# Optimization experiments

Hardware: AMD Instinct MI355X
Metric: run time of the kernel (lower is better)

The kernel has to match this reference:

```python
import jax, jax.numpy as jnp
import numpy as np

B, S, D = 8, 1024, 1024
H = 16
DH = D // H
DFF = 4096
L = 2
EPS = 1e-6


def setup_inputs() -> dict:
    key = jax.random.key(0)
    ks = jax.random.split(key, 12)
    sc = 0.02
    x = jax.random.normal(ks[0], (B, S, D), dtype=jnp.float32)
    # causal mask: 1 where position j > i (masked), broadcast over batch/head
    mask = jnp.triu(jnp.ones((S, S), dtype=jnp.float32), k=1)[None, None]
    Wq = jax.random.normal(ks[1], (L, D, D), dtype=jnp.float32) * sc
    Wk = jax.random.normal(ks[2], (L, D, D), dtype=jnp.float32) * sc
    Wv = jax.random.normal(ks[3], (L, D, D), dtype=jnp.float32) * sc
    Wo = jax.random.normal(ks[4], (L, D, D), dtype=jnp.float32) * sc
    bq = jnp.zeros((L, D), jnp.float32)
    bk = jnp.zeros((L, D), jnp.float32)
    bv = jnp.zeros((L, D), jnp.float32)
    bo = jnp.zeros((L, D), jnp.float32)
    W1 = jax.random.normal(ks[5], (L, D, DFF), dtype=jnp.float32) * sc
    b1 = jnp.zeros((L, DFF), jnp.float32)
    W2 = jax.random.normal(ks[6], (L, DFF, D), dtype=jnp.float32) * sc
    b2 = jnp.zeros((L, D), jnp.float32)
    ln1_g = jnp.ones((L, D), jnp.float32)
    ln1_b = jnp.zeros((L, D), jnp.float32)
    ln2_g = jnp.ones((L, D), jnp.float32)
    ln2_b = jnp.zeros((L, D), jnp.float32)
    return dict(x=x, mask=mask, Wq=Wq, bq=bq, Wk=Wk, bk=bk, Wv=Wv, bv=bv,
                Wo=Wo, bo=bo, W1=W1, b1=b1, W2=W2, b2=b2,
                ln1_g=ln1_g, ln1_b=ln1_b, ln2_g=ln2_g, ln2_b=ln2_b)


def layer_norm(x, g, b):
    mu = jnp.mean(x, axis=-1, keepdims=True)
    var = jnp.mean(jnp.square(x - mu), axis=-1, keepdims=True)
    return (x - mu) * jax.lax.rsqrt(var + EPS) * g + b


def reference(x, mask, Wq, bq, Wk, bk, Wv, bv, Wo, bo, W1, b1, W2, b2,
              ln1_g, ln1_b, ln2_g, ln2_b):
    scale = 1.0 / jnp.sqrt(jnp.float32(DH))
    for l in range(L):
        # --- multi-head attention (inference mode: no dropout) ---
        q = (x @ Wq[l] + bq[l]).reshape(B, S, H, DH).transpose(0, 2, 1, 3)
        k = (x @ Wk[l] + bk[l]).reshape(B, S, H, DH).transpose(0, 2, 1, 3)
        v = (x @ Wv[l] + bv[l]).reshape(B, S, H, DH).transpose(0, 2, 1, 3)
        sim = jnp.einsum('bhqd,bhkd->bhqk', q, k) * scale + mask * (-1e9)
        attn = jax.nn.softmax(sim, axis=-1)
        o = jnp.einsum('bhqk,bhkd->bhqd', attn, v)
        o = o.transpose(0, 2, 1, 3).reshape(B, S, D)
        o = o @ Wo[l] + bo[l]
        x = layer_norm(o + x, ln1_g[l], ln1_b[l])
        # --- feed-forward network ---
        h = jax.nn.relu(x @ W1[l] + b1[l])
        f = h @ W2[l] + b2[l]
        x = layer_norm(x + f, ln2_g[l], ln2_b[l])
    return x
```

## Files before the change

### kernel.cpp

```cpp
#include <hip/hip_runtime.h>

typedef __attribute__((ext_vector_type(8))) short bf16x8;
typedef __attribute__((ext_vector_type(4))) float f32x4;
typedef unsigned short ushort_t;
typedef unsigned int uint32;

#define DEV __device__ __forceinline__

DEV ushort_t f2bf(float f) {
    uint32 u = __float_as_uint(f);
    uint32 r = (u + 0x7FFFu + ((u >> 16) & 1u)) >> 16;
    return (ushort_t)r;
}
DEV float bf2f(ushort_t h) { return __uint_as_float(((uint32)h) << 16); }

#define MFMA16(a, b, c) __builtin_amdgcn_mfma_f32_16x16x32_bf16((a), (b), (c), 0, 0, 0)

DEV void gload_lds16(const void* g, void* l) {
    __builtin_amdgcn_global_load_lds((const __attribute__((address_space(1))) void*)g,
                                     (__attribute__((address_space(3))) void*)l,
                                     16, 0, 0);
}

__global__ __launch_bounds__(256) void init_x(const float* __restrict__ xin,
                                              ushort_t* __restrict__ xr, int n4) {
    int i = blockIdx.x * 256 + threadIdx.x;
    if (i >= n4) return;
    float4 v = ((const float4*)xin)[i];
    ushort4 h;
    h.x = f2bf(v.x); h.y = f2bf(v.y); h.z = f2bf(v.z); h.w = f2bf(v.w);
    ((ushort4*)xr)[i] = h;
}

__global__ __launch_bounds__(256) void transpose_all(const float* __restrict__ Wq,
                                                     const float* __restrict__ Wk,
                                                     const float* __restrict__ Wv,
                                                     const float* __restrict__ Wo,
                                                     const float* __restrict__ W1,
                                                     const float* __restrict__ W2,
                                                     ushort_t* __restrict__ wqkvT,
                                                     ushort_t* __restrict__ woT,
                                                     ushort_t* __restrict__ w1T,
                                                     ushort_t* __restrict__ w2T) {
    const int l = blockIdx.y;
    const int t = blockIdx.x;
    const float* src;
    ushort_t* dst;
    int K, N, ktile, ntile;
    if (t < 4096) {
        const int which = t >> 10, tile = t & 1023;
        K = 1024; N = 1024; ktile = tile >> 5; ntile = tile & 31;
        const size_t o1 = (size_t)l * 1048576;
        if (which == 0)      { src = Wq + o1; dst = wqkvT + (size_t)l * 3145728; }
        else if (which == 1) { src = Wk + o1; dst = wqkvT + (size_t)l * 3145728 + 1048576; }
        else if (which == 2) { src = Wv + o1; dst = wqkvT + (size_t)l * 3145728 + 2097152; }
        else                 { src = Wo + o1; dst = woT + o1; }
    } else if (t < 8192) {
        const int tile = t - 4096;
        K = 1024; N = 4096; ktile = tile >> 7; ntile = tile & 127;
        src = W1 + (size_t)l * 4194304; dst = w1T + (size_t)l * 4194304;
    } else {
        const int tile = t - 8192;
        K = 4096; N = 1024; ktile = tile >> 5; ntile = tile & 31;
        src = W2 + (size_t)l * 4194304; dst = w2T + (size_t)l * 4194304;
    }
    __shared__ float tilebuf[32][33];
    const int tx = threadIdx.x, ty = threadIdx.y;
    const int nt = ntile * 32, kt = ktile * 32;
#pragma unroll
    for (int j = 0; j < 4; ++j)
        tilebuf[ty + j * 8][tx] = src[(size_t)(kt + ty + j * 8) * N + nt + tx];
    __syncthreads();
#pragma unroll
    for (int j = 0; j < 4; ++j)
        dst[(size_t)(nt + ty + j * 8) * K + kt + tx] = f2bf(tilebuf[tx][ty + j * 8]);
}

template <int BM, int MODE, int RELU>
__global__ __launch_bounds__(512, 2) void gemm8p(const ushort_t* __restrict__ A,
                                                 const ushort_t* __restrict__ BT,
                                                 const float* __restrict__ bias,
                                                 void* __restrict__ Cout,
                                                 int M, int N, int K, int gx,
                                                 ushort_t* __restrict__ qout,
                                                 ushort_t* __restrict__ kout,
                                                 ushort_t* __restrict__ vtout,
                                                 const float* __restrict__ bq,
                                                 const float* __restrict__ bk,
                                                 const float* __restrict__ bv) {
    constexpr int AH = BM / 128;
    constexpr int MREP = BM / 32;
    constexpr int PHASES = (BM == 128) ? 2 : 4;
    __shared__ ushort_t lds[2][(BM + 256) * 64];

    const int nwg = gridDim.x;
    const int q8 = nwg >> 3, r8 = nwg & 7;
    const int xcd = blockIdx.x & 7, idx = blockIdx.x >> 3;
    const int swz = (xcd < r8 ? xcd * (q8 + 1) : r8 * (q8 + 1) + (xcd - r8) * q8) + idx;
    const int gchunk = gx * 8;
    const int grp = swz / gchunk, rem = swz % gchunk;
    const int byi = grp * 8 + (rem & 7);
    const int bxi = rem >> 3;

    const int tid = threadIdx.x;
    const int w = tid >> 6, lane = tid & 63;
    const int wr = w >> 2, wc = w & 3;
    const int lr = lane & 15, lh = lane >> 4;
    const int row0 = byi * BM, col0 = bxi * 256;

    f32x4 acc[MREP][4] = {};

    const ushort_t* __restrict__ Ab = A + (size_t)row0 * K;
    const ushort_t* __restrict__ Bb = BT + (size_t)col0 * K;
    const int nt = K >> 6;

    const int r8l = lane >> 3;
    const int cu = (lane & 7) ^ r8l;
    const int so = w * 1024 + lane * 8;

    const ushort_t* aS[AH][2];
    const ushort_t* bS[2][2];
#pragma unroll
    for (int h2 = 0; h2 < AH; ++h2)
#pragma unroll
        for (int i = 0; i < 2; ++i)
            aS[h2][i] = Ab + (size_t)(h2 * 128 + (w * 2 + i) * 8 + r8l) * K + cu * 8;
#pragma unroll
    for (int h2 = 0; h2 < 2; ++h2)
#pragma unroll
        for (int i = 0; i < 2; ++i)
            bS[h2][i] = Bb + (size_t)(h2 * 128 + (w * 2 + i) * 8 + r8l) * K + cu * 8;

    auto stageA = [&](int buf, int h2) {
#pragma unroll
        for (int i = 0; i < 2; ++i) {
            gload_lds16(aS[h2][i], &lds[buf][h2 * 8192 + so + i * 512]);
            aS[h2][i] += 64;
        }
    };
    auto stageB = [&](int buf, int h2) {
#pragma unroll
        for (int i = 0; i < 2; ++i) {
            gload_lds16(bS[h2][i], &lds[buf][BM * 64 + h2 * 8192 + so + i * 512]);
            bS[h2][i] += 64;
        }
    };

    int boff[4][2];
#pragma unroll
    for (int ni = 0; ni < 4; ++ni) {
        const int br = wc * 64 + ni * 16 + lr;
        const int rr = br & 127, bh2 = br >> 7;
#pragma unroll
        for (int ks = 0; ks < 2; ++ks)
            boff[ni][ks] = BM * 64 + bh2 * 8192 + rr * 64 + (((ks * 4 + lh) ^ (rr & 7)) * 8);
    }
    int aoff[MREP][2];
#pragma unroll
    for (int mi = 0; mi < MREP; ++mi) {
        const int fr = wr * (BM / 2) + mi * 16 + lr;
        const int rr = fr & 127, fh = fr >> 7;
#pragma unroll
        for (int ks = 0; ks < 2; ++ks)
            aoff[mi][ks] = fh * 8192 + rr * 64 + (((ks * 4 + lh) ^ (rr & 7)) * 8);
    }

    stageB(0, 0); stageB(0, 1);
    stageA(0, 0); if (AH == 2) stageA(0, 1);
    stageB(1, 0); stageB(1, 1);
    asm volatile("s_waitcnt vmcnt(4)" ::: "memory");
    __builtin_amdgcn_sched_barrier(0);
    __builtin_amdgcn_s_barrier();

    for (int t2 = 0; t2 < nt; t2 += 2) {
#pragma unroll
        for (int ti = 0; ti < 2; ++ti) {
            const int t = t2 + ti;
            bf16x8 bfr[2][4];
#pragma unroll
            for (int p = 0; p < PHASES; ++p) {
                const int ks = p & 1;
                const int mh = (PHASES == 4) ? (p >> 1) : 0;
                if (mh == 0) {
#pragma unroll
                    for (int ni = 0; ni < 4; ++ni)
                        bfr[ks][ni] = *(const bf16x8*)&lds[ti][boff[ni][ks]];
                }
                bf16x8 af[4];
#pragma unroll
                for (int mm = 0; mm < 4; ++mm)
                    af[mm] = *(const bf16x8*)&lds[ti][aoff[mh * 4 + mm][ks]];
                if (PHASES == 4) {
                    if (p == 0) { if (t + 1 < nt) stageA(1 - ti, 0); }
                    else if (p == 1) { if (AH == 2 && t + 1 < nt) stageA(1 - ti, 1); }
                    else if (p == 2) { if (t + 2 < nt) stageB(ti, 0); }
                    else {
                        if (t + 2 < nt) {
                            stageB(ti, 1);
                            asm volatile("s_waitcnt vmcnt(4)" ::: "memory");
                        } else if (t + 1 < nt) {
                            asm volatile("s_waitcnt vmcnt(0)" ::: "memory");
                        }
                    }
                } else {
                    if (p == 0) { if (t + 1 < nt) stageA(1 - ti, 0); }
                    else {
                        if (t + 2 < nt) {
                            stageB(ti, 0);
                            stageB(ti, 1);
                            asm volatile("s_waitcnt vmcnt(4)" ::: "memory");
                        } else if (t + 1 < nt) {
                            asm volatile("s_waitcnt vmcnt(0)" ::: "memory");
                        }
                    }
                }
                __builtin_amdgcn_sched_barrier(0);
                __builtin_amdgcn_s_barrier();
                asm volatile("s_waitcnt lgkmcnt(0)" ::: "memory");
                __builtin_amdgcn_sched_barrier(0);
                __builtin_amdgcn_s_setprio(1);
#pragma unroll
                for (int mm = 0; mm < 4; ++mm)
#pragma unroll
                    for (int ni = 0; ni < 4; ++ni)
                        acc[mh * 4 + mm][ni] = MFMA16(af[mm], bfr[ks][ni], acc[mh * 4 + mm][ni]);
                __builtin_amdgcn_s_setprio(0);
                __builtin_amdgcn_sched_barrier(0);
                __builtin_amdgcn_s_barrier();
            }
        }
    }
    (void)M;

    if (MODE == 2 && col0 >= 2048) {
        ushort_t* vb = &lds[0][0] + w * 4096;
        const int hglob = (col0 - 2048 + wc * 64) >> 6;
        const int bidx = row0 >> 10;
        const int srow0 = (row0 & 1023) + wr * 64;
#pragma unroll
        for (int mi = 0; mi < MREP; ++mi) {
#pragma unroll
            for (int ni = 0; ni < 4; ++ni) {
                const int dd = ni * 16 + lr;
                const float bvv = bv[(hglob << 6) + dd];
                ushort4 h4;
                h4.x = f2bf(acc[mi][ni][0] + bvv);
                h4.y = f2bf(acc[mi][ni][1] + bvv);
                h4.z = f2bf(acc[mi][ni][2] + bvv);
                h4.w = f2bf(acc[mi][ni][3] + bvv);
                const int sb = mi * 32 + lh * 8;
                *(ushort4*)((char*)vb + dd * 128 + (sb ^ ((dd & 3) << 4))) = h4;
            }
        }
        const int ddl = lane >> 3, s8 = lane & 7;
#pragma unroll
        for (int j = 0; j < 8; ++j) {
            const int dd = j * 8 + ddl;
            bf16x8 rowv = *(const bf16x8*)((char*)vb + dd * 128 + ((s8 * 16) ^ ((dd & 3) << 4)));
            *(bf16x8*)&vtout[(((size_t)(bidx * 16 + hglob) * 64 + dd) << 10) + srow0 + s8 * 8] = rowv;
        }
    } else {
#pragma unroll
        for (int mi = 0; mi < MREP; ++mi) {
#pragma unroll
            for (int ni = 0; ni < 4; ++ni) {
                const int col = col0 + wc * 64 + ni * 16 + lr;
                const int rowb = row0 + wr * (BM / 2) + mi * 16 + lh * 4;
                if (MODE == 2) {
                    if (col < 1024) {
                        const float bvv = bq[col];
#pragma unroll
                        for (int r = 0; r < 4; ++r)
                            qout[(size_t)(rowb + r) * 1024 + col] = f2bf((acc[mi][ni][r] + bvv) * 0.125f);
                    } else {
                        const int c = col - 1024;
                        const float bvv = bk[c];
#pragma unroll
                        for (int r = 0; r < 4; ++r)
                            kout[(size_t)(rowb + r) * 1024 + c] = f2bf(acc[mi][ni][r] + bvv);
                    }
                } else {
                    const float bvv = bias[col];
#pragma unroll
                    for (int r = 0; r < 4; ++r) {
                        float val = acc[mi][ni][r] + bvv;
                        if (RELU) val = fmaxf(val, 0.f);
                        ((ushort_t*)Cout)[(size_t)(rowb + r) * N + col] = f2bf(val);
                    }
                }
            }
        }
    }
}

__global__ __launch_bounds__(256) void attn_kernel(const ushort_t* __restrict__ q,
                                                   const ushort_t* __restrict__ k,
                                                   const ushort_t* __restrict__ vt,
                                                   ushort_t* __restrict__ o) {
    __shared__ ushort_t ktile[128 * 64];
    __shared__ ushort_t vtile[64 * 128];
    __shared__ ushort_t p_lds[4][16 * 128];

    const int bh = blockIdx.x;
    const int b = bh >> 4, h = bh & 15;
    const int qt = blockIdx.y;
    const int tid = threadIdx.x, w = tid >> 6, lane = tid & 63;
    const int lr = lane & 15, lh = lane >> 4;
    const int qbase = qt * 64 + w * 16;
    const size_t headoff = (size_t)b * 1024 * 1024 + h * 64;
    const size_t vhead = (size_t)(b * 16 + h) << 16;

    bf16x8 qf[2];
#pragma unroll
    for (int ks = 0; ks < 2; ++ks)
        qf[ks] = *(const bf16x8*)&q[headoff + (size_t)(qbase + lr) * 1024 + ks * 32 + lh * 8];

    f32x4 oacc[4] = {};
    float m[4] = {-INFINITY, -INFINITY, -INFINITY, -INFINITY};
    float ls[4] = {0.f, 0.f, 0.f, 0.f};

    const int srow = tid >> 3;
    const int scol8 = (tid & 7) * 8;
    char* const kbase = (char*)ktile;
    char* const vbase = (char*)vtile;
    const int kswzb = (scol8 * 2) ^ ((srow & 7) << 4);
    const int vswzr = ((srow & 15) << 4);
    const ushort_t* kg = k + headoff + (size_t)srow * 1024 + scol8;
    const ushort_t* vg = vt + vhead + (size_t)srow * 1024 + scol8;

    const int jmaxw = qbase + 15;
    const int jend = qt * 64 + 63;

    bf16x8 sk[4], sv[4];
#pragma unroll
    for (int p = 0; p < 4; ++p) sk[p] = *(const bf16x8*)&kg[(size_t)(p * 32) * 1024];
#pragma unroll
    for (int p = 0; p < 2; ++p)
#pragma unroll
        for (int kh = 0; kh < 2; ++kh)
            sv[p * 2 + kh] = *(const bf16x8*)&vg[(size_t)(p * 32) * 1024 + kh * 64];

    for (int j0 = 0; j0 <= jend; j0 += 128) {
        __syncthreads();
#pragma unroll
        for (int p = 0; p < 4; ++p)
            *(bf16x8*)(kbase + (srow + 32 * p) * 128 + kswzb) = sk[p];
#pragma unroll
        for (int p = 0; p < 2; ++p)
#pragma unroll
            for (int kh = 0; kh < 2; ++kh)
                *(bf16x8*)(vbase + (srow + 32 * p) * 256 + ((kh * 128 + scol8 * 2) ^ vswzr)) = sv[p * 2 + kh];
        __syncthreads();
        if (j0 + 128 <= jend) {
#pragma unroll
            for (int p = 0; p < 4; ++p)
                sk[p] = *(const bf16x8*)&kg[(size_t)(j0 + 128 + p * 32) * 1024];
#pragma unroll
            for (int p = 0; p < 2; ++p)
#pragma unroll
                for (int kh = 0; kh < 2; ++kh)
                    sv[p * 2 + kh] = *(const bf16x8*)&vg[(size_t)(p * 32) * 1024 + j0 + 128 + kh * 64];
        }

        if (j0 <= jmaxw) {
            f32x4 s[8] = {};
#pragma unroll
            for (int kt = 0; kt < 8; ++kt) {
                const int krow = kt * 16 + lr;
                const int rswz = ((krow & 7) << 4);
#pragma unroll
                for (int ks = 0; ks < 2; ++ks) {
                    bf16x8 kf = *(const bf16x8*)(kbase + krow * 128 + ((ks * 64 + lh * 16) ^ rswz));
                    s[kt] = MFMA16(qf[ks], kf, s[kt]);
                }
            }
            if (j0 + 127 > qbase) {
#pragma unroll
                for (int kt = 0; kt < 8; ++kt)
#pragma unroll
                    for (int r = 0; r < 4; ++r)
                        s[kt][r] = ((j0 + kt * 16 + lr) <= (qbase + lh * 4 + r)) ? s[kt][r] : -1e9f;
            }
#pragma unroll
            for (int r = 0; r < 4; ++r) {
                float pm = fmaxf(fmaxf(fmaxf(s[0][r], s[1][r]), fmaxf(s[2][r], s[3][r])),
                                 fmaxf(fmaxf(s[4][r], s[5][r]), fmaxf(s[6][r], s[7][r])));
                pm = fmaxf(pm, __shfl_xor(pm, 1, 16));
                pm = fmaxf(pm, __shfl_xor(pm, 2, 16));
                pm = fmaxf(pm, __shfl_xor(pm, 4, 16));
                pm = fmaxf(pm, __shfl_xor(pm, 8, 16));
                const float mn = fmaxf(m[r], pm);
                const float corr = __expf(m[r] - mn);
                m[r] = mn;
                float ps = 0.f;
#pragma unroll
                for (int kt = 0; kt < 8; ++kt) {
                    const float pv = __expf(s[kt][r] - mn);
                    s[kt][r] = pv;
                    ps += pv;
                }
                ps += __shfl_xor(ps, 1, 16);
                ps += __shfl_xor(ps, 2, 16);
                ps += __shfl_xor(ps, 4, 16);
                ps += __shfl_xor(ps, 8, 16);
                ls[r] = ls[r] * corr + ps;
                oacc[0][r] *= corr; oacc[1][r] *= corr;
                oacc[2][r] *= corr; oacc[3][r] *= corr;
            }
            char* const pb = (char*)p_lds[w];
#pragma unroll
            for (int r = 0; r < 4; ++r) {
                const int qrow = lh * 4 + r;
                const int qswz = ((qrow & 15) << 4);
#pragma unroll
                for (int kt = 0; kt < 8; ++kt)
                    *(ushort_t*)(pb + qrow * 256 + ((kt * 32 + lr * 2) ^ qswz)) = f2bf(s[kt][r]);
            }
            const int pswz = ((lr & 15) << 4);
            bf16x8 pa[4];
#pragma unroll
            for (int ks = 0; ks < 4; ++ks)
                pa[ks] = *(const bf16x8*)(pb + lr * 256 + ((ks * 64 + lh * 16) ^ pswz));
#pragma unroll
            for (int dt = 0; dt < 4; ++dt) {
                const int vrow = dt * 16 + lr;
                const int vswz = ((vrow & 15) << 4);
#pragma unroll
                for (int ks = 0; ks < 4; ++ks) {
                    bf16x8 vf = *(const bf16x8*)(vbase + vrow * 256 + ((ks * 64 + lh * 16) ^ vswz));
                    oacc[dt] = MFMA16(pa[ks], vf, oacc[dt]);
                }
            }
        }
    }

    float inv[4];
#pragma unroll
    for (int r = 0; r < 4; ++r) inv[r] = 1.f / ls[r];
#pragma unroll
    for (int dt = 0; dt < 4; ++dt)
#pragma unroll
        for (int r = 0; r < 4; ++r) {
            const int row = qbase + lh * 4 + r;
            o[headoff + (size_t)row * 1024 + dt * 16 + lr] = f2bf(oacc[dt][r] * inv[r]);
        }
}

template <int LAST>
__global__ __launch_bounds__(256) void add_ln(const ushort_t* __restrict__ t,
                                              ushort_t* __restrict__ xr,
                                              const float* __restrict__ g,
                                              const float* __restrict__ bb,
                                              float* __restrict__ out) {
    const int row = blockIdx.x, tid = threadIdx.x;
    const int lane = tid & 63, w = tid >> 6;
    const size_t base = (size_t)row * 1024;
    ushort4 tv = ((const ushort4*)(t + base))[tid];
    ushort4 xv = ((const ushort4*)(xr + base))[tid];
    float v0 = bf2f(tv.x) + bf2f(xv.x), v1 = bf2f(tv.y) + bf2f(xv.y);
    float v2 = bf2f(tv.z) + bf2f(xv.z), v3 = bf2f(tv.w) + bf2f(xv.w);
    float s = v0 + v1 + v2 + v3;
    float sq = v0 * v0 + v1 * v1 + v2 * v2 + v3 * v3;
#pragma unroll
    for (int off = 32; off >= 1; off >>= 1) {
        s += __shfl_xor(s, off);
        sq += __shfl_xor(sq, off);
    }
    __shared__ float red[8];
    if (lane == 0) { red[w] = s; red[4 + w] = sq; }
    __syncthreads();
    s = red[0] + red[1] + red[2] + red[3];
    sq = red[4] + red[5] + red[6] + red[7];
    const float mu = s * (1.f / 1024.f);
    const float var = sq * (1.f / 1024.f) - mu * mu;
    const float rs = rsqrtf(var + 1e-6f);
    float4 gv = ((const float4*)g)[tid];
    float4 bv = ((const float4*)bb)[tid];
    float y0 = (v0 - mu) * rs * gv.x + bv.x;
    float y1 = (v1 - mu) * rs * gv.y + bv.y;
    float y2 = (v2 - mu) * rs * gv.z + bv.z;
    float y3 = (v3 - mu) * rs * gv.w + bv.w;
    if (LAST) {
        float4 yo; yo.x = y0; yo.y = y1; yo.z = y2; yo.w = y3;
        ((float4*)(out + base))[tid] = yo;
    } else {
        ushort4 hh;
        hh.x = f2bf(y0); hh.y = f2bf(y1); hh.z = f2bf(y2); hh.w = f2bf(y3);
        ((ushort4*)(xr + base))[tid] = hh;
    }
}

extern "C" void kernel_launch(void* const* d_in, const int* in_sizes, int n_in,
                              void* d_out, int out_size, void* d_ws, size_t ws_size,
                              hipStream_t stream) {
    (void)in_sizes; (void)n_in; (void)out_size; (void)ws_size;
    const int B = 8, S = 1024, D = 1024, DFF = 4096, L = 2;
    const int M = B * S;

    const float* x_in = (const float*)d_in[0];
    const float* Wq = (const float*)d_in[2];
    const float* bq = (const float*)d_in[3];
    const float* Wk = (const float*)d_in[4];
    const float* bk = (const float*)d_in[5];
    const float* Wv = (const float*)d_in[6];
    const float* bv = (const float*)d_in[7];
    const float* Wo = (const float*)d_in[8];
    const float* bo = (const float*)d_in[9];
    const float* W1 = (const float*)d_in[10];
    const float* b1 = (const float*)d_in[11];
    const float* W2 = (const float*)d_in[12];
    const float* b2 = (const float*)d_in[13];
    const float* ln1g = (const float*)d_in[14];
    const float* ln1b = (const float*)d_in[15];
    const float* ln2g = (const float*)d_in[16];
    const float* ln2b = (const float*)d_in[17];

    float* out = (float*)d_out;
    char* ws = (char*)d_ws;
    const size_t MB = 1024 * 1024;
    ushort_t* wqkvT = (ushort_t*)(ws + 0 * MB);
    ushort_t* woT = (ushort_t*)(ws + 12 * MB);
    ushort_t* w1T = (ushort_t*)(ws + 16 * MB);
    ushort_t* w2T = (ushort_t*)(ws + 32 * MB);
    ushort_t* xr  = (ushort_t*)(ws + 48 * MB);
    ushort_t* qb  = (ushort_t*)(ws + 64 * MB);
    ushort_t* kb  = (ushort_t*)(ws + 80 * MB);
    ushort_t* vtb = (ushort_t*)(ws + 96 * MB);
    ushort_t* ob  = (ushort_t*)(ws + 112 * MB);
    ushort_t* hb  = (ushort_t*)(ws + 64 * MB);
    ushort_t* tb  = (ushort_t*)(ws + 128 * MB);

    init_x<<<M * D / 4 / 256, 256, 0, stream>>>(x_in, xr, M * D / 4);
    transpose_all<<<dim3(12288, L), dim3(32, 8), 0, stream>>>(
        Wq, Wk, Wv, Wo, W1, W2, wqkvT, woT, w1T, w2T);

    for (int l = 0; l < L; ++l) {
        const size_t wOff = (size_t)l * D * D;
        const size_t bOff = (size_t)l * D;
        gemm8p<128, 2, 0><<<dim3(768), 512, 0, stream>>>(
            xr, wqkvT + (size_t)l * 3 * D * D, nullptr, nullptr, M, 3 * D, D, 12,
            qb, kb, vtb, bq + bOff, bk + bOff, bv + bOff);
        attn_kernel<<<dim3(B * 16, S / 64), 256, 0, stream>>>(qb, kb, vtb, ob);
        gemm8p<128, 1, 0><<<dim3(256), 512, 0, stream>>>(
            ob, woT + wOff, bo + bOff, tb, M, D, D, 4,
            nullptr, nullptr, nullptr, nullptr, nullptr, nullptr);
        add_ln<0><<<M, 256, 0, stream>>>(tb, xr, ln1g + bOff, ln1b + bOff, nullptr);
        gemm8p<256, 1, 1><<<dim3(512), 512, 0, stream>>>(
            xr, w1T + (size_t)l * D * DFF, b1 + (size_t)l * DFF, hb, M, DFF, D, 16,
            nullptr, nullptr, nullptr, nullptr, nullptr, nullptr);
        gemm8p<128, 1, 0><<<dim3(256), 512, 0, stream>>>(
            hb, w2T + (size_t)l * DFF * D, b2 + bOff, tb, M, D, DFF, 4,
            nullptr, nullptr, nullptr, nullptr, nullptr, nullptr);
        if (l == L - 1)
            add_ln<1><<<M, 256, 0, stream>>>(tb, xr, ln2g + bOff, ln2b + bOff, out);
        else
            add_ln<0><<<M, 256, 0, stream>>>(tb, xr, ln2g + bOff, ln2b + bOff, nullptr);
    }
}
```

Before: 657.5 us.

## Add BK=32 K-tile variant of GEMM and use it for QKV projection

Adds a BK template parameter to the pipelined bf16 GEMM, with a new K-depth-32 path that has its own swizzled LDS layout, a one-load-per-thread staging scheme and a two-phase M-split schedule. The QKV projection (768 workgroups) now uses BK=32, which halves its LDS footprint per buffer while the other GEMMs keep BK=64. The aim is to shrink LDS use and improve occupancy or latency hiding on the QKV GEMM. The cost is twice as many barriers per unit of K work and shallower MFMA bursts between syncs.

```diff
diff --git a/kernel.cpp b/kernel.cpp
--- a/kernel.cpp
+++ b/kernel.cpp
@@ -6,6 +6,7 @@
 typedef unsigned int uint32;
 
 #define DEV __device__ __forceinline__
+#define SBAR() __builtin_amdgcn_sched_barrier(0)
 
 DEV ushort_t f2bf(float f) {
     uint32 u = __float_as_uint(f);
@@ -76,7 +77,7 @@
         dst[(size_t)(nt + ty + j * 8) * K + kt + tx] = f2bf(tilebuf[tx][ty + j * 8]);
 }
 
-template <int BM, int MODE, int RELU>
+template <int BM, int BK, int MODE, int RELU>
 __global__ __launch_bounds__(512, 2) void gemm8p(const ushort_t* __restrict__ A,
                                                  const ushort_t* __restrict__ BT,
                                                  const float* __restrict__ bias,
@@ -90,8 +91,12 @@
                                                  const float* __restrict__ bv) {
     constexpr int AH = BM / 128;
     constexpr int MREP = BM / 32;
+    constexpr int MH = MREP / 2;
     constexpr int PHASES = (BM == 128) ? 2 : 4;
-    __shared__ ushort_t lds[2][(BM + 256) * 64];
+    constexpr int BUFSZ = (BM + 256) * BK;
+    constexpr int LDSSZ = (MODE == 2 && 2 * BUFSZ < 32768) ? 32768 : 2 * BUFSZ;
+    constexpr int HALF = 128 * BK;
+    __shared__ ushort_t ldsf[LDSSZ];
 
     const int nwg = gridDim.x;
     const int q8 = nwg >> 3, r8 = nwg & 7;
@@ -112,37 +117,57 @@
 
     const ushort_t* __restrict__ Ab = A + (size_t)row0 * K;
     const ushort_t* __restrict__ Bb = BT + (size_t)col0 * K;
-    const int nt = K >> 6;
+    const int nt = K / BK;
 
     const int r8l = lane >> 3;
-    const int cu = (lane & 7) ^ r8l;
-    const int so = w * 1024 + lane * 8;
+    const int cu64 = (lane & 7) ^ r8l;
+    const int so64 = w * 1024 + lane * 8;
+    const int srow32 = tid >> 2;
+    const int cu32 = (tid & 3) ^ ((srow32 >> 1) & 3);
 
     const ushort_t* aS[AH][2];
     const ushort_t* bS[2][2];
 #pragma unroll
     for (int h2 = 0; h2 < AH; ++h2)
 #pragma unroll
-        for (int i = 0; i < 2; ++i)
-            aS[h2][i] = Ab + (size_t)(h2 * 128 + (w * 2 + i) * 8 + r8l) * K + cu * 8;
+        for (int i = 0; i < 2; ++i) {
+            if (BK == 64)
+                aS[h2][i] = Ab + (size_t)(h2 * 128 + (w * 2 + i) * 8 + r8l) * K + cu64 * 8;
+            else
+                aS[h2][i] = Ab + (size_t)(h2 * 128 + srow32) * K + cu32 * 8;
+        }
 #pragma unroll
     for (int h2 = 0; h2 < 2; ++h2)
 #pragma unroll
-        for (int i = 0; i < 2; ++i)
-            bS[h2][i] = Bb + (size_t)(h2 * 128 + (w * 2 + i) * 8 + r8l) * K + cu * 8;
+        for (int i = 0; i < 2; ++i) {
+            if (BK == 64)
+                bS[h2][i] = Bb + (size_t)(h2 * 128 + (w * 2 + i) * 8 + r8l) * K + cu64 * 8;
+            else
+                bS[h2][i] = Bb + (size_t)(h2 * 128 + srow32) * K + cu32 * 8;
+        }
 
     auto stageA = [&](int buf, int h2) {
-#pragma unroll
-        for (int i = 0; i < 2; ++i) {
-            gload_lds16(aS[h2][i], &lds[buf][h2 * 8192 + so + i * 512]);
-            aS[h2][i] += 64;
+        if (BK == 64) {
+#pragma unroll
+            for (int i = 0; i < 2; ++i) {
+                gload_lds16(aS[h2][i], &ldsf[buf * BUFSZ + h2 * HALF + so64 + i * 512]);
+                aS[h2][i] += 64;
+            }
+        } else {
+            gload_lds16(aS[h2][0], &ldsf[buf * BUFSZ + h2 * HALF + tid * 8]);
+            aS[h2][0] += 32;
         }
     };
     auto stageB = [&](int buf, int h2) {
-#pragma unroll
-        for (int i = 0; i < 2; ++i) {
-            gload_lds16(bS[h2][i], &lds[buf][BM * 64 + h2 * 8192 + so + i * 512]);
-            bS[h2][i] += 64;
+        if (BK == 64) {
+#pragma unroll
+            for (int i = 0; i < 2; ++i) {
+                gload_lds16(bS[h2][i], &ldsf[buf * BUFSZ + BM * BK + h2 * HALF + so64 + i * 512]);
+                bS[h2][i] += 64;
+            }
+        } else {
+            gload_lds16(bS[h2][0], &ldsf[buf * BUFSZ + BM * BK + h2 * HALF + tid * 8]);
+            bS[h2][0] += 32;
         }
     };
 
@@ -152,8 +177,12 @@
         const int br = wc * 64 + ni * 16 + lr;
         const int rr = br & 127, bh2 = br >> 7;
 #pragma unroll
-        for (int ks = 0; ks < 2; ++ks)
-            boff[ni][ks] = BM * 64 + bh2 * 8192 + rr * 64 + (((ks * 4 + lh) ^ (rr & 7)) * 8);
+        for (int ks = 0; ks < 2; ++ks) {
+            if (BK == 64)
+                boff[ni][ks] = BM * 64 + bh2 * HALF + rr * 64 + (((ks * 4 + lh) ^ (rr & 7)) * 8);
+            else
+                boff[ni][ks] = BM * 32 + bh2 * HALF + rr * 32 + ((lh ^ ((rr >> 1) & 3)) * 8);
+        }
     }
     int aoff[MREP][2];
 #pragma unroll
@@ -161,79 +190,134 @@
         const int fr = wr * (BM / 2) + mi * 16 + lr;
         const int rr = fr & 127, fh = fr >> 7;
 #pragma unroll
-        for (int ks = 0; ks < 2; ++ks)
-            aoff[mi][ks] = fh * 8192 + rr * 64 + (((ks * 4 + lh) ^ (rr & 7)) * 8);
+        for (int ks = 0; ks < 2; ++ks) {
+            if (BK == 64)
+                aoff[mi][ks] = fh * HALF + rr * 64 + (((ks * 4 + lh) ^ (rr & 7)) * 8);
+            else
+                aoff[mi][ks] = fh * HALF + rr * 32 + ((lh ^ ((rr >> 1) & 3)) * 8);
+        }
     }
 
     stageB(0, 0); stageB(0, 1);
     stageA(0, 0); if (AH == 2) stageA(0, 1);
     stageB(1, 0); stageB(1, 1);
-    asm volatile("s_waitcnt vmcnt(4)" ::: "memory");
-    __builtin_amdgcn_sched_barrier(0);
+    if (BK == 64) asm volatile("s_waitcnt vmcnt(4)" ::: "memory");
+    else          asm volatile("s_waitcnt vmcnt(2)" ::: "memory");
+    SBAR();
     __builtin_amdgcn_s_barrier();
 
     for (int t2 = 0; t2 < nt; t2 += 2) {
 #pragma unroll
         for (int ti = 0; ti < 2; ++ti) {
             const int t = t2 + ti;
-            bf16x8 bfr[2][4];
-#pragma unroll
-            for (int p = 0; p < PHASES; ++p) {
-                const int ks = p & 1;
-                const int mh = (PHASES == 4) ? (p >> 1) : 0;
-                if (mh == 0) {
-#pragma unroll
-                    for (int ni = 0; ni < 4; ++ni)
-                        bfr[ks][ni] = *(const bf16x8*)&lds[ti][boff[ni][ks]];
-                }
-                bf16x8 af[4];
-#pragma unroll
-                for (int mm = 0; mm < 4; ++mm)
-                    af[mm] = *(const bf16x8*)&lds[ti][aoff[mh * 4 + mm][ks]];
-                if (PHASES == 4) {
-                    if (p == 0) { if (t + 1 < nt) stageA(1 - ti, 0); }
-                    else if (p == 1) { if (AH == 2 && t + 1 < nt) stageA(1 - ti, 1); }
-                    else if (p == 2) { if (t + 2 < nt) stageB(ti, 0); }
-                    else {
-                        if (t + 2 < nt) {
-                            stageB(ti, 1);
-                            asm volatile("s_waitcnt vmcnt(4)" ::: "memory");
-                        } else if (t + 1 < nt) {
-                            asm volatile("s_waitcnt vmcnt(0)" ::: "memory");
+            if (BK == 64) {
+                bf16x8 bfr[2][4];
+#pragma unroll
+                for (int p = 0; p < PHASES; ++p) {
+                    const int ks = p & 1;
+                    const int mh = (PHASES == 4) ? (p >> 1) : 0;
+                    if (mh == 0) {
+#pragma unroll
+                        for (int ni = 0; ni < 4; ++ni)
+                            bfr[ks][ni] = *(const bf16x8*)&ldsf[ti * BUFSZ + boff[ni][ks]];
+                    }
+                    bf16x8 af[4];
+#pragma unroll
+                    for (int mm = 0; mm < 4; ++mm)
+                        af[mm] = *(const bf16x8*)&ldsf[ti * BUFSZ + aoff[mh * 4 + mm][ks]];
+                    if (PHASES == 4) {
+                        if (p == 0) { if (t + 1 < nt) stageA(1 - ti, 0); }
+                        else if (p == 1) { if (AH == 2 && t + 1 < nt) stageA(1 - ti, 1); }
+                        else if (p == 2) { if (t + 2 < nt) stageB(ti, 0); }
+                        else {
+                            if (t + 2 < nt) {
+                                stageB(ti, 1);
+                                asm volatile("s_waitcnt vmcnt(4)" ::: "memory");
+                            } else if (t + 1 < nt) {
+                                asm volatile("s_waitcnt vmcnt(0)" ::: "memory");
+                            }
+                        }
+                    } else {
+                        if (p == 0) { if (t + 1 < nt) stageA(1 - ti, 0); }
+                        else {
+                            if (t + 2 < nt) {
+                                stageB(ti, 0);
+                                stageB(ti, 1);
+                                asm volatile("s_waitcnt vmcnt(4)" ::: "memory");
+                            } else if (t + 1 < nt) {
+                                asm volatile("s_waitcnt vmcnt(0)" ::: "memory");
+                            }
                         }
                     }
-                } else {
-                    if (p == 0) { if (t + 1 < nt) stageA(1 - ti, 0); }
-                    else {
-                        if (t + 2 < nt) {
-                            stageB(ti, 0);
-                            stageB(ti, 1);
-                            asm volatile("s_waitcnt vmcnt(4)" ::: "memory");
-                        } else if (t + 1 < nt) {
-                            asm volatile("s_waitcnt vmcnt(0)" ::: "memory");
-                        }
-                    }
+                    SBAR();
+                    __builtin_amdgcn_s_barrier();
+                    asm volatile("s_waitcnt lgkmcnt(0)" ::: "memory");
+                    SBAR();
+                    __builtin_amdgcn_s_setprio(1);
+#pragma unroll
+                    for (int mm = 0; mm < 4; ++mm)
+#pragma unroll
+                        for (int ni = 0; ni < 4; ++ni)
+                            acc[mh * 4 + mm][ni] = MFMA16(af[mm], bfr[ks][ni], acc[mh * 4 + mm][ni]);
+                    __builtin_amdgcn_s_setprio(0);
+                    SBAR();
+                    __builtin_amdgcn_s_barrier();
                 }
-                __builtin_amdgcn_sched_barrier(0);
+            } else {
+                bf16x8 bfr[4], af[MREP];
+#pragma unroll
+                for (int ni = 0; ni < 4; ++ni)
+                    bfr[ni] = *(const bf16x8*)&ldsf[ti * BUFSZ + boff[ni][0]];
+#pragma unroll
+                for (int mi = 0; mi < MH; ++mi)
+                    af[mi] = *(const bf16x8*)&ldsf[ti * BUFSZ + aoff[mi][0]];
+                if (t + 1 < nt) {
+                    stageA(1 - ti, 0);
+                    if (AH == 2) stageA(1 - ti, 1);
+                }
+                SBAR();
                 __builtin_amdgcn_s_barrier();
                 asm volatile("s_waitcnt lgkmcnt(0)" ::: "memory");
-                __builtin_amdgcn_sched_barrier(0);
+                SBAR();
                 __builtin_amdgcn_s_setprio(1);
 #pragma unroll
-                for (int mm = 0; mm < 4; ++mm)
+                for (int mi = 0; mi < MH; ++mi)
 #pragma unroll
                     for (int ni = 0; ni < 4; ++ni)
-                        acc[mh * 4 + mm][ni] = MFMA16(af[mm], bfr[ks][ni], acc[mh * 4 + mm][ni]);
+                        acc[mi][ni] = MFMA16(af[mi], bfr[ni], acc[mi][ni]);
                 __builtin_amdgcn_s_setprio(0);
-                __builtin_amdgcn_sched_barrier(0);
+                SBAR();
                 __builtin_amdgcn_s_barrier();
+#pragma unroll
+                for (int mi = MH; mi < MREP; ++mi)
+                    af[mi] = *(const bf16x8*)&ldsf[ti * BUFSZ + aoff[mi][0]];
+                if (t + 2 < nt) {
+                    stageB(ti, 0);
+                    stageB(ti, 1);
+                    asm volatile("s_waitcnt vmcnt(2)" ::: "memory");
+                } else if (t + 1 < nt) {
+                    asm volatile("s_waitcnt vmcnt(0)" ::: "memory");
+                }
+                SBAR();
+                __builtin_amdgcn_s_barrier();
+                asm volatile("s_waitcnt lgkmcnt(0)" ::: "memory");
+                SBAR();
+                __builtin_amdgcn_s_setprio(1);
+#pragma unroll
+                for (int mi = MH; mi < MREP; ++mi)
+#pragma unroll
+                    for (int ni = 0; ni < 4; ++ni)
+                        acc[mi][ni] = MFMA16(af[mi], bfr[ni], acc[mi][ni]);
+                __builtin_amdgcn_s_setprio(0);
+                SBAR();
+                __builtin_amdgcn_s_barrier();
             }
         }
     }
     (void)M;
 
     if (MODE == 2 && col0 >= 2048) {
-        ushort_t* vb = &lds[0][0] + w * 4096;
+        ushort_t* vb = ldsf + w * 4096;
         const int hglob = (col0 - 2048 + wc * 64) >> 6;
         const int bidx = row0 >> 10;
         const int srow0 = (row0 & 1023) + wr * 64;
@@ -537,18 +621,18 @@
     for (int l = 0; l < L; ++l) {
         const size_t wOff = (size_t)l * D * D;
         const size_t bOff = (size_t)l * D;
-        gemm8p<128, 2, 0><<<dim3(768), 512, 0, stream>>>(
+        gemm8p<128, 32, 2, 0><<<dim3(768), 512, 0, stream>>>(
             xr, wqkvT + (size_t)l * 3 * D * D, nullptr, nullptr, M, 3 * D, D, 12,
             qb, kb, vtb, bq + bOff, bk + bOff, bv + bOff);
         attn_kernel<<<dim3(B * 16, S / 64), 256, 0, stream>>>(qb, kb, vtb, ob);
-        gemm8p<128, 1, 0><<<dim3(256), 512, 0, stream>>>(
+        gemm8p<128, 64, 1, 0><<<dim3(256), 512, 0, stream>>>(
             ob, woT + wOff, bo + bOff, tb, M, D, D, 4,
             nullptr, nullptr, nullptr, nullptr, nullptr, nullptr);
         add_ln<0><<<M, 256, 0, stream>>>(tb, xr, ln1g + bOff, ln1b + bOff, nullptr);
-        gemm8p<256, 1, 1><<<dim3(512), 512, 0, stream>>>(
+        gemm8p<256, 64, 1, 1><<<dim3(512), 512, 0, stream>>>(
             xr, w1T + (size_t)l * D * DFF, b1 + (size_t)l * DFF, hb, M, DFF, D, 16,
             nullptr, nullptr, nullptr, nullptr, nullptr, nullptr);
-        gemm8p<128, 1, 0><<<dim3(256), 512, 0, stream>>>(
+        gemm8p<128, 64, 1, 0><<<dim3(256), 512, 0, stream>>>(
             hb, w2T + (size_t)l * DFF * D, b2 + bOff, tb, M, D, DFF, 4,
             nullptr, nullptr, nullptr, nullptr, nullptr, nullptr);
         if (l == L - 1)
```

Measured after the change: 651.8 us (median of 3 runs). Within noise of the previous version (-0.9%).
